# Performance work log

Hardware: AMD Instinct MI355X
Metric: run time of the kernel (lower is better)

## Reference

```python
import math
import jax, jax.numpy as jnp
import numpy as np

B, S, D = 2, 2048, 1024
H, DK = 16, 64
NUM_BUCKETS = 32
MAX_DISTANCE = 128


def _relative_position_bucket(relative_position, num_buckets=NUM_BUCKETS, max_distance=MAX_DISTANCE):
    # bidirectional=True branch (encoder / non-causal)
    n = -relative_position
    num_buckets = num_buckets // 2
    ret = (n < 0).astype(jnp.int32) * num_buckets
    n = jnp.abs(n)
    max_exact = num_buckets // 2
    is_small = n < max_exact
    # guard log(0); masked out by is_small anyway
    n_safe = jnp.maximum(n, 1).astype(jnp.float32)
    val_if_large = max_exact + (
        jnp.log(n_safe / max_exact) / math.log(max_distance / max_exact) * (num_buckets - max_exact)
    ).astype(jnp.int32)
    val_if_large = jnp.minimum(val_if_large, num_buckets - 1)
    return ret + jnp.where(is_small, n, val_if_large)


def setup_inputs() -> dict:
    key = jax.random.key(0)
    ks = jax.random.split(key, 6)
    std_q = (D * DK) ** -0.5
    std = D ** -0.5
    return {
        "x": jax.random.normal(ks[0], (B, S, D), jnp.float32),
        "q_w": jax.random.normal(ks[1], (H * DK, D), jnp.float32) * std_q,
        "k_w": jax.random.normal(ks[2], (H * DK, D), jnp.float32) * std,
        "v_w": jax.random.normal(ks[3], (H * DK, D), jnp.float32) * std,
        "o_w": jax.random.normal(ks[4], (D, H * DK), jnp.float32) * ((H * DK) ** -0.5),
        "rel_bias": jax.random.normal(ks[5], (NUM_BUCKETS, H), jnp.float32) * std,
    }


def reference(x, q_w, k_w, v_w, o_w, rel_bias):
    b, s, _ = x.shape
    # project and split heads: [B, H, S, DK]
    def proj(w):
        return (x @ w.T).reshape(b, s, H, DK).transpose(0, 2, 1, 3)
    q, k, v = proj(q_w), proj(k_w), proj(v_w)

    # T5-style unscaled attention scores: [B, H, Sq, Sk]
    scores = jnp.einsum("bhqd,bhkd->bhqk", q, k)

    # bucketed relative-position bias
    ctx = jnp.arange(s)[:, None]
    mem = jnp.arange(s)[None, :]
    rp_bucket = _relative_position_bucket(mem - ctx)  # [S, S]
    bias = rel_bias[rp_bucket]                        # [S, S, H]
    bias = bias.transpose(2, 0, 1)[None]              # [1, H, S, S]
    scores = scores + bias

    attn = jax.nn.softmax(scores, axis=-1)
    ctx_out = jnp.einsum("bhqk,bhkd->bhqd", attn, v)
    ctx_out = ctx_out.transpose(0, 2, 1, 3).reshape(b, s, H * DK)
    return ctx_out @ o_w.T
```

## Files before the change

kernel.cpp:

```cpp
#include <hip/hip_runtime.h>
#include <stdint.h>


typedef unsigned short u16;
typedef __attribute__((ext_vector_type(8))) short short8;
typedef __attribute__((ext_vector_type(4))) float float4v;
typedef __attribute__((ext_vector_type(4))) u16 ushort4v;
typedef __attribute__((ext_vector_type(4))) uint32_t uint4v;

typedef __attribute__((address_space(1))) void void_g;
typedef __attribute__((address_space(3))) void void_l;

#define L2E 1.4426950408889634f

__device__ __forceinline__ u16 f2b(float f) {
  union { float f; uint32_t u; } v; v.f = f;
  uint32_t r = (v.u + 0x7fffu + ((v.u >> 16) & 1u)) >> 16;
  return (u16)r;
}
__device__ __forceinline__ u16 f2b_fast(float f) {
  union { float f; uint32_t u; } v; v.f = f;
  return (u16)((v.u + 0x8000u) >> 16);
}
__device__ __forceinline__ uint32_t cvt_pk_bf16(float lo, float hi) {
  uint32_t r;
  asm("v_cvt_pk_bf16_f32 %0, %1, %2" : "=v"(r) : "v"(lo), "v"(hi));
  return r;
}

__global__ void cvt_all(const float* __restrict__ x,  const float* __restrict__ qw,
                        const float* __restrict__ kw, const float* __restrict__ vw,
                        const float* __restrict__ ow, const float* __restrict__ rel_bias,
                        u16* __restrict__ xb, u16* __restrict__ wqkv, u16* __restrict__ owb,
                        float* __restrict__ biasT) {
  int bi = blockIdx.x;
  if (bi >= 8192) {
    int idx = (bi - 8192) * 256 + threadIdx.x;
    int h = idx >> 12, t = idx & 4095;
    if (t > 4094) { biasT[h * 4096 + 4095] = -1.0e4f; return; }
    int d = t - 2047;
    int n = -d;
    int ret = (n < 0) ? 16 : 0;
    int na = (n < 0) ? -n : n;
    int bucket;
    if (na < 8) {
      bucket = ret + na;
    } else {
      float v = logf((float)na / 8.0f) / logf(16.0f) * 8.0f;
      int vi = 8 + (int)v;
      bucket = ret + (vi > 15 ? 15 : vi);
    }
    biasT[h * 4096 + t] = (rel_bias[bucket * 16 + h] - 8.0f) * L2E;
    return;
  }
  int i = bi * 256 + threadIdx.x;
  const float* s; u16* d; int off;
  if (i < 1048576)      { s = x;  d = xb;              off = i; }
  else if (i < 1310720) { s = qw; d = wqkv;            off = i - 1048576; }
  else if (i < 1572864) { s = kw; d = wqkv + 1048576;  off = i - 1310720; }
  else if (i < 1835008) { s = vw; d = wqkv + 2097152;  off = i - 1572864; }
  else                  { s = ow; d = owb;             off = i - 1835008; }
  float4v v = ((const float4v*)s)[off];
  ushort4v o;
  o.x = f2b(v.x); o.y = f2b(v.y); o.z = f2b(v.z); o.w = f2b(v.w);
  ((ushort4v*)d)[off] = o;
}

__global__ __launch_bounds__(256, 2)
void gemm_qkv(const u16* __restrict__ A, const u16* __restrict__ W,
              u16* __restrict__ qkb, u16* __restrict__ vTp) {
  const int K = 1024;
  __shared__ __align__(16) char SM[65536];
  const int tid = threadIdx.x;
  const int wid = tid >> 6;
  const int lane = tid & 63;
  const int row16 = lane & 15, oct = lane >> 4;
  const int lin = blockIdx.x + blockIdx.y * 32;
  const int V = (lin & 7) * 96 + (lin >> 3);
  const int bx = V & 31, by = V >> 5;
  const int tm = bx * 128, tn = by * 128;
  const int wm = (wid & 1) * 64, wn = (wid >> 1) * 64;
  const int srow = lane >> 2;
  const int sc = (lane & 3) * 8;
  float4v acc[4][4] = {};

#define STAGE_QKV(buf, k0)                                                            \
  {                                                                                   \
    u16* Ad = (u16*)(SM + (buf) * 32768);                                             \
    u16* Bd = (u16*)(SM + (buf) * 32768 + 16384);                                     \
    _Pragma("unroll")                                                                 \
    for (int i = 0; i < 4; i++) {                                                     \
      const int idx = i * 4 + wid;                                                    \
      const int kk = idx & 1;                                                         \
      const int rb = idx >> 1;                                                        \
      const int r = rb * 16 + srow;                                                   \
      const int c = kk * 32 + sc;                                                     \
      __builtin_amdgcn_global_load_lds((void_g*)(A + (size_t)(tm + r) * K + (k0) + c),\
                                       (void_l*)(Ad + (kk * 128 + rb * 16) * 32), 16, 0, 0); \
      __builtin_amdgcn_global_load_lds((void_g*)(W + (size_t)(tn + r) * K + (k0) + c),\
                                       (void_l*)(Bd + (kk * 128 + rb * 16) * 32), 16, 0, 0); \
    }                                                                                 \
  }

  STAGE_QKV(0, 0);
  __syncthreads();
  for (int t = 0; t < 16; t++) {
    if (t + 1 < 16) STAGE_QKV((t + 1) & 1, (t + 1) * 64);
    const u16* As = (const u16*)(SM + (t & 1) * 32768);
    const u16* Bs = As + 8192;
#pragma unroll
    for (int kk = 0; kk < 2; kk++) {
      short8 af[4], bfr[4];
#pragma unroll
      for (int mi = 0; mi < 4; mi++)
        af[mi] = *(const short8*)(As + (kk * 128 + wm + mi * 16 + row16) * 32 + oct * 8);
#pragma unroll
      for (int ni = 0; ni < 4; ni++)
        bfr[ni] = *(const short8*)(Bs + (kk * 128 + wn + ni * 16 + row16) * 32 + oct * 8);
#pragma unroll
      for (int mi = 0; mi < 4; mi++)
#pragma unroll
        for (int ni = 0; ni < 4; ni++)
          acc[mi][ni] = __builtin_amdgcn_mfma_f32_16x16x32_bf16(af[mi], bfr[ni], acc[mi][ni], 0, 0, 0);
    }
    __syncthreads();
  }

  if (tn < 2048) {
    u16* Es = (u16*)SM;
#pragma unroll
    for (int mi = 0; mi < 4; mi++)
#pragma unroll
      for (int ni = 0; ni < 4; ni++)
#pragma unroll
        for (int r = 0; r < 4; r++)
          Es[(wm + mi * 16 + oct * 4 + r) * 136 + wn + ni * 16 + row16] = f2b(acc[mi][ni][r]);
    __syncthreads();
#pragma unroll
    for (int it = 0; it < 8; it++) {
      int idx = it * 256 + tid;
      int row = idx >> 4, c = idx & 15;
      short8 v = *(const short8*)(Es + row * 136 + c * 8);
      *(short8*)(qkb + (size_t)(tm + row) * 2048 + tn + c * 8) = v;
    }
  } else {
    const int h0 = (tn - 2048) >> 6;
    const int b = tm >> 11;
    const int s0 = tm & 2047;
#pragma unroll
    for (int ni = 0; ni < 4; ni++) {
      const int dg = wn + ni * 16 + row16;
      const int head = h0 + (dg >> 6), d = dg & 63;
      u16* vdst = vTp + ((size_t)((b * 16 + head) * 64 + d)) * 2048 + s0 + wm + oct * 8;
#pragma unroll
      for (int bb = 0; bb < 2; bb++) {
        uint4v pw;
        pw.x = cvt_pk_bf16(acc[2 * bb][ni][0], acc[2 * bb][ni][1]);
        pw.y = cvt_pk_bf16(acc[2 * bb][ni][2], acc[2 * bb][ni][3]);
        pw.z = cvt_pk_bf16(acc[2 * bb + 1][ni][0], acc[2 * bb + 1][ni][1]);
        pw.w = cvt_pk_bf16(acc[2 * bb + 1][ni][2], acc[2 * bb + 1][ni][3]);
        *(uint4v*)(vdst + bb * 32) = pw;
      }
    }
  }
}

__global__ __launch_bounds__(256, 2)
void gemm_out(const u16* __restrict__ A, const u16* __restrict__ W,
              float* __restrict__ C) {
  const int K = 1024, N = 1024;
  __shared__ __align__(16) char SM[49152];
  const int tid = threadIdx.x;
  const int wid = tid >> 6;
  const int lane = tid & 63;
  const int row16 = lane & 15, oct = lane >> 4;
  const int tm = blockIdx.x * 64, tn = blockIdx.y * 128;
  const int wm = (wid & 1) * 32, wn = (wid >> 1) * 64;
  const int srow = lane >> 2;
  const int sc = (lane & 3) * 8;
  float4v acc[2][4] = {};

#define STAGE_OUT(buf, k0)                                                            \
  {                                                                                   \
    u16* Ad = (u16*)(SM + (buf) * 24576);                                             \
    u16* Bd = (u16*)(SM + (buf) * 24576 + 8192);                                      \
    _Pragma("unroll")                                                                 \
    for (int i = 0; i < 2; i++) {                                                     \
      const int idx = i * 4 + wid;                                                    \
      const int kk = idx & 1;                                                         \
      const int rb = idx >> 1;                                                        \
      const int r = rb * 16 + srow;                                                   \
      const int c = kk * 32 + sc;                                                     \
      __builtin_amdgcn_global_load_lds((void_g*)(A + (size_t)(tm + r) * K + (k0) + c),\
                                       (void_l*)(Ad + (kk * 64 + rb * 16) * 32), 16, 0, 0); \
    }                                                                                 \
    _Pragma("unroll")                                                                 \
    for (int i = 0; i < 4; i++) {                                                     \
      const int idx = i * 4 + wid;                                                    \
      const int kk = idx & 1;                                                         \
      const int rb = idx >> 1;                                                        \
      const int r = rb * 16 + srow;                                                   \
      const int c = kk * 32 + sc;                                                     \
      __builtin_amdgcn_global_load_lds((void_g*)(W + (size_t)(tn + r) * K + (k0) + c),\
                                       (void_l*)(Bd + (kk * 128 + rb * 16) * 32), 16, 0, 0); \
    }                                                                                 \
  }

  STAGE_OUT(0, 0);
  __syncthreads();
  for (int t = 0; t < 16; t++) {
    if (t + 1 < 16) STAGE_OUT((t + 1) & 1, (t + 1) * 64);
    const u16* As = (const u16*)(SM + (t & 1) * 24576);
    const u16* Bs = As + 4096;
#pragma unroll
    for (int kk = 0; kk < 2; kk++) {
      short8 af[2], bfr[4];
#pragma unroll
      for (int mi = 0; mi < 2; mi++)
        af[mi] = *(const short8*)(As + (kk * 64 + wm + mi * 16 + row16) * 32 + oct * 8);
#pragma unroll
      for (int ni = 0; ni < 4; ni++)
        bfr[ni] = *(const short8*)(Bs + (kk * 128 + wn + ni * 16 + row16) * 32 + oct * 8);
#pragma unroll
      for (int mi = 0; mi < 2; mi++)
#pragma unroll
        for (int ni = 0; ni < 4; ni++)
          acc[mi][ni] = __builtin_amdgcn_mfma_f32_16x16x32_bf16(af[mi], bfr[ni], acc[mi][ni], 0, 0, 0);
    }
    __syncthreads();
  }
  float* Ef = (float*)SM;
#pragma unroll
  for (int mi = 0; mi < 2; mi++)
#pragma unroll
    for (int ni = 0; ni < 4; ni++)
#pragma unroll
      for (int r = 0; r < 4; r++)
        Ef[(wm + mi * 16 + oct * 4 + r) * 132 + wn + ni * 16 + row16] = acc[mi][ni][r];
  __syncthreads();
#pragma unroll
  for (int it = 0; it < 8; it++) {
    int idx = it * 256 + tid;
    int row = idx >> 5, c = idx & 31;
    float4v v = *(const float4v*)(Ef + row * 132 + c * 4);
    *(float4v*)(C + (size_t)(tm + row) * N + tn + c * 4) = v;
  }
}

__global__ __launch_bounds__(256, 2)
void flash_attn(const u16* __restrict__ qkb, const u16* __restrict__ vTp,
                const float* __restrict__ biasT, u16* __restrict__ ctx) {
  const int S = 2048, LDQ = 2048;
  const int lin = blockIdx.x + (blockIdx.y << 4) + (blockIdx.z << 8);
  const int V = (lin & 7) * 64 + (lin >> 3);
  const int qt0 = (V & 15) * 128;
  const int h = (V >> 4) & 15, b = V >> 8;
  const int tid = threadIdx.x, wid = tid >> 6, lane = tid & 63;
  const int row16 = lane & 15, oct = lane >> 4;

  __shared__ __align__(16) float biasS[2176];
  __shared__ __align__(16) u16 Ks[2][64][40];
  __shared__ __align__(16) u16 Vts[2][64][40];

  {
    const float* bsrc = biasT + h * 4096 + (1920 - qt0);
    for (int i = tid; i < 544; i += 256)
      ((float4v*)biasS)[i] = ((const float4v*)bsrc)[i];
  }
  const float bias_neg = biasT[h * 4096];
  const float bias_pos = biasT[h * 4096 + 4094];

  const u16* qbase = qkb + ((size_t)b * S + qt0 + wid * 32) * LDQ + h * 64;
  short8 qf[2][2];
#pragma unroll
  for (int f = 0; f < 2; f++)
#pragma unroll
    for (int hd = 0; hd < 2; hd++)
      qf[f][hd] = *(const short8*)(qbase + (size_t)(f * 16 + row16) * LDQ + hd * 32 + oct * 8);

  float4v l_acc[2] = {};
  float4v o_acc[2][4] = {};
  const short8 ones = {0x3F80, 0x3F80, 0x3F80, 0x3F80, 0x3F80, 0x3F80, 0x3F80, 0x3F80};

  const int sr = lane >> 2, c8 = (lane & 3) * 8;
  const int srow = wid * 16 + sr;
  const u16* Kst = qkb + 1024 + ((size_t)b * S + srow) * LDQ + c8 + h * 64;
  const u16* Vst = vTp + ((size_t)(b * 16 + h) * 64 + srow) * 2048 + c8;

  short8 kreg[2], vreg[2];
#pragma unroll
  for (int hd = 0; hd < 2; hd++) kreg[hd] = *(const short8*)(Kst + hd * 32);
#pragma unroll
  for (int ks = 0; ks < 2; ks++) vreg[ks] = *(const short8*)(Vst + ks * 32);

  for (int kt = 0; kt < S; kt += 64) {
    __syncthreads();
#pragma unroll
    for (int hd = 0; hd < 2; hd++) *(short8*)&Ks[hd][srow][c8] = kreg[hd];
#pragma unroll
    for (int ks = 0; ks < 2; ks++) *(short8*)&Vts[ks][srow][c8] = vreg[ks];
    __syncthreads();

    if (kt + 64 < S) {
#pragma unroll
      for (int hd = 0; hd < 2; hd++)
        kreg[hd] = *(const short8*)(Kst + (size_t)(kt + 64) * LDQ + hd * 32);
#pragma unroll
      for (int ks = 0; ks < 2; ks++)
        vreg[ks] = *(const short8*)(Vst + (kt + 64) + ks * 32);
    }

    short8 kf[4][2];
#pragma unroll
    for (int st = 0; st < 4; st++)
#pragma unroll
      for (int hd = 0; hd < 2; hd++)
        kf[st][hd] = *(const short8*)&Ks[hd][st * 16 + row16][oct * 8];

    float4v sc[2][4];
    __builtin_amdgcn_s_setprio(1);
#pragma unroll
    for (int f = 0; f < 2; f++)
#pragma unroll
      for (int st = 0; st < 4; st++) {
        float4v s = {};
        s = __builtin_amdgcn_mfma_f32_16x16x32_bf16(kf[st][0], qf[f][0], s, 0, 0, 0);
        s = __builtin_amdgcn_mfma_f32_16x16x32_bf16(kf[st][1], qf[f][1], s, 0, 0, 0);
        sc[f][st] = s;
      }
    __builtin_amdgcn_s_setprio(0);

    short8 vf[2][4];
#pragma unroll
    for (int ks = 0; ks < 2; ks++)
#pragma unroll
      for (int ni = 0; ni < 4; ni++)
        vf[ks][ni] = *(const short8*)&Vts[ks][ni * 16 + row16][oct * 8];

    const int dk = kt - qt0;
    const bool far = (dk >= 256) || (dk <= -192);
    if (far) {
      const float bc = (dk > 0) ? bias_pos : bias_neg;
#pragma unroll
      for (int f = 0; f < 2; f++)
#pragma unroll
        for (int st = 0; st < 4; st++)
#pragma unroll
          for (int r = 0; r < 4; r++)
            sc[f][st][r] = __builtin_amdgcn_exp2f(__builtin_fmaf(sc[f][st][r], L2E, bc));
    } else {
#pragma unroll
      for (int f = 0; f < 2; f++) {
        const int basef = kt + oct * 4 - wid * 32 - f * 16 - row16 + 127;
#pragma unroll
        for (int st = 0; st < 4; st++)
#pragma unroll
          for (int r = 0; r < 4; r++)
            sc[f][st][r] = __builtin_amdgcn_exp2f(
                __builtin_fmaf(sc[f][st][r], L2E, biasS[basef + st * 16 + r]));
      }
    }

#pragma unroll
    for (int f = 0; f < 2; f++) {
#pragma unroll
      for (int ks = 0; ks < 2; ks++) {
        uint4v pw;
        pw.x = cvt_pk_bf16(sc[f][2 * ks][0], sc[f][2 * ks][1]);
        pw.y = cvt_pk_bf16(sc[f][2 * ks][2], sc[f][2 * ks][3]);
        pw.z = cvt_pk_bf16(sc[f][2 * ks + 1][0], sc[f][2 * ks + 1][1]);
        pw.w = cvt_pk_bf16(sc[f][2 * ks + 1][2], sc[f][2 * ks + 1][3]);
        short8 pf = __builtin_bit_cast(short8, pw);
        __builtin_amdgcn_s_setprio(1);
#pragma unroll
        for (int ni = 0; ni < 4; ni++)
          o_acc[f][ni] = __builtin_amdgcn_mfma_f32_16x16x32_bf16(pf, vf[ks][ni], o_acc[f][ni], 0, 0, 0);
        l_acc[f] = __builtin_amdgcn_mfma_f32_16x16x32_bf16(pf, ones, l_acc[f], 0, 0, 0);
        __builtin_amdgcn_s_setprio(0);
      }
    }
  }

#pragma unroll
  for (int f = 0; f < 2; f++) {
    float linv[4];
#pragma unroll
    for (int r = 0; r < 4; r++)
      linv[r] = 1.0f / l_acc[f][r];
    const size_t orow = (size_t)b * S + qt0 + wid * 32 + f * 16 + oct * 4;
#pragma unroll
    for (int ni = 0; ni < 4; ni++)
#pragma unroll
      for (int r = 0; r < 4; r++)
        ctx[(orow + r) * 1024 + h * 64 + ni * 16 + row16] = f2b_fast(o_acc[f][ni][r] * linv[r]);
  }
}

extern "C" void kernel_launch(void* const* d_in, const int* in_sizes, int n_in,
                              void* d_out, int out_size, void* d_ws, size_t ws_size,
                              hipStream_t stream) {
  const float* x        = (const float*)d_in[0];
  const float* q_w      = (const float*)d_in[1];
  const float* k_w      = (const float*)d_in[2];
  const float* v_w      = (const float*)d_in[3];
  const float* o_w      = (const float*)d_in[4];
  const float* rel_bias = (const float*)d_in[5];

  char* ws = (char*)d_ws;
  u16*   xb    = (u16*)(ws);
  u16*   wqkv  = (u16*)(ws + 8388608);
  u16*   owb   = (u16*)(ws + 14680064);
  u16*   qkb   = (u16*)(ws + 16777216);
  u16*   vTp   = (u16*)(ws + 33554432);
  u16*   ctxb  = (u16*)(ws + 41943040);
  float* biasT = (float*)(ws + 50331648);

  cvt_all<<<8448, 256, 0, stream>>>(x, q_w, k_w, v_w, o_w, rel_bias,
                                    xb, wqkv, owb, biasT);

  dim3 g1(4096 / 128, 3072 / 128);
  gemm_qkv<<<g1, 256, 0, stream>>>(xb, wqkv, qkb, vTp);

  dim3 g2(2048 / 128, 16, 2);
  flash_attn<<<g2, 256, 0, stream>>>(qkb, vTp, biasT, ctxb);

  dim3 g3(4096 / 64, 1024 / 128);
  gemm_out<<<g3, 256, 0, stream>>>(ctxb, owb, (float*)d_out);
}
```

Baseline: 177.7 us.

## Single-buffer QKV GEMM staging to fit three blocks per CU

The QKV projection GEMM drops its double-buffered LDS pipeline and uses one 32KB stage buffer, plus padding for the epilogue. The launch bound rises from 2 to 3 blocks per CU. Prefetching the next K tile while computing the current one is lost, so each iteration now waits on its own load, and more resident blocks have to hide that latency instead.

```diff
diff --git a/kernel.cpp b/kernel.cpp
--- a/kernel.cpp
+++ b/kernel.cpp
@@ -66,11 +66,13 @@
   ((ushort4v*)d)[off] = o;
 }
 
-__global__ __launch_bounds__(256, 2)
+__global__ __launch_bounds__(256, 3)
 void gemm_qkv(const u16* __restrict__ A, const u16* __restrict__ W,
               u16* __restrict__ qkb, u16* __restrict__ vTp) {
   const int K = 1024;
-  __shared__ __align__(16) char SM[65536];
+  __shared__ __align__(16) char SM[34816];
+  u16* As = (u16*)SM;
+  u16* Bs = (u16*)(SM + 16384);
   const int tid = threadIdx.x;
   const int wid = tid >> 6;
   const int lane = tid & 63;
@@ -83,31 +85,21 @@
   const int srow = lane >> 2;
   const int sc = (lane & 3) * 8;
   float4v acc[4][4] = {};
-
-#define STAGE_QKV(buf, k0)                                                            \
-  {                                                                                   \
-    u16* Ad = (u16*)(SM + (buf) * 32768);                                             \
-    u16* Bd = (u16*)(SM + (buf) * 32768 + 16384);                                     \
-    _Pragma("unroll")                                                                 \
-    for (int i = 0; i < 4; i++) {                                                     \
-      const int idx = i * 4 + wid;                                                    \
-      const int kk = idx & 1;                                                         \
-      const int rb = idx >> 1;                                                        \
-      const int r = rb * 16 + srow;                                                   \
-      const int c = kk * 32 + sc;                                                     \
-      __builtin_amdgcn_global_load_lds((void_g*)(A + (size_t)(tm + r) * K + (k0) + c),\
-                                       (void_l*)(Ad + (kk * 128 + rb * 16) * 32), 16, 0, 0); \
-      __builtin_amdgcn_global_load_lds((void_g*)(W + (size_t)(tn + r) * K + (k0) + c),\
-                                       (void_l*)(Bd + (kk * 128 + rb * 16) * 32), 16, 0, 0); \
-    }                                                                                 \
-  }
-
-  STAGE_QKV(0, 0);
-  __syncthreads();
-  for (int t = 0; t < 16; t++) {
-    if (t + 1 < 16) STAGE_QKV((t + 1) & 1, (t + 1) * 64);
-    const u16* As = (const u16*)(SM + (t & 1) * 32768);
-    const u16* Bs = As + 8192;
+  for (int k0 = 0; k0 < K; k0 += 64) {
+    __syncthreads();
+#pragma unroll
+    for (int i = 0; i < 4; i++) {
+      const int idx = i * 4 + wid;
+      const int kk = idx & 1;
+      const int rb = idx >> 1;
+      const int r = rb * 16 + srow;
+      const int c = kk * 32 + sc;
+      __builtin_amdgcn_global_load_lds((void_g*)(A + (size_t)(tm + r) * K + k0 + c),
+                                       (void_l*)(As + (kk * 128 + rb * 16) * 32), 16, 0, 0);
+      __builtin_amdgcn_global_load_lds((void_g*)(W + (size_t)(tn + r) * K + k0 + c),
+                                       (void_l*)(Bs + (kk * 128 + rb * 16) * 32), 16, 0, 0);
+    }
+    __syncthreads();
 #pragma unroll
     for (int kk = 0; kk < 2; kk++) {
       short8 af[4], bfr[4];
@@ -123,11 +115,11 @@
         for (int ni = 0; ni < 4; ni++)
           acc[mi][ni] = __builtin_amdgcn_mfma_f32_16x16x32_bf16(af[mi], bfr[ni], acc[mi][ni], 0, 0, 0);
     }
-    __syncthreads();
   }
 
   if (tn < 2048) {
     u16* Es = (u16*)SM;
+    __syncthreads();
 #pragma unroll
     for (int mi = 0; mi < 4; mi++)
 #pragma unroll
```

New measurement: 172.0 us. 3.2% less time.
